# Kernel tuning notes

Measured on AMD Instinct MI355X. Metric: run time of the kernel, lower is better.

Reference implementation:

```python
import jax, jax.numpy as jnp
import numpy as np

N, C, NIRR, E = 2048, 128, 9, 10          # nodes, channels, sum(2l+1) of input irreps, num elements
DOUT = (1, 3)                              # output irrep dims for 128x0e + 128x1o
K3, K2, K1 = 4, 3, 2                       # number of CG paths per correlation order


def setup_inputs() -> dict:
    key = jax.random.key(0)
    ks = jax.random.split(key, 24)
    inp = {
        'node_feats': jax.random.normal(ks[0], (N, C, NIRR), jnp.float32),
        'node_attrs': jax.nn.one_hot(jax.random.randint(ks[1], (N,), 0, E), E, dtype=jnp.float32),
        'sc': jax.random.normal(ks[2], (N, C * sum(DOUT)), jnp.float32),
    }
    i = 3
    for li, d in enumerate(DOUT):
        # U tensors: fixed (buffer) generalized CG coupling tensors; sparse in e3nn,
        # here random dense stand-ins with the exact same shapes / contraction structure.
        inp[f'u3_l{li}'] = 0.1 * jax.random.normal(ks[i + 0], (d, NIRR, NIRR, NIRR, K3), jnp.float32)
        inp[f'u2_l{li}'] = 0.1 * jax.random.normal(ks[i + 1], (d, NIRR, NIRR, K2), jnp.float32)
        inp[f'u1_l{li}'] = 0.1 * jax.random.normal(ks[i + 2], (d, NIRR, K1), jnp.float32)
        s3, s2, s1 = 1.0 / np.sqrt(K3 * C), 1.0 / np.sqrt(K2 * C), 1.0 / np.sqrt(K1 * C)
        inp[f'w3_l{li}'] = s3 * jax.random.normal(ks[i + 3], (E, K3, C), jnp.float32)
        inp[f'w2_l{li}'] = s2 * jax.random.normal(ks[i + 4], (E, K2, C), jnp.float32)
        inp[f'w1_l{li}'] = s1 * jax.random.normal(ks[i + 5], (E, K1, C), jnp.float32)
        i += 6
    inp['lin_w0'] = jax.random.normal(ks[i], (C, C), jnp.float32)
    inp['lin_w1'] = jax.random.normal(ks[i + 1], (C, C), jnp.float32)
    return inp


def _contraction(x, y, u3, u2, u1, w3, w2, w1):
    # MACE Contraction: correlation-3 nested CG contraction for one output irrep.
    # x: [N,C,n], y: [N,E] one-hot, u_nu: [d, n*nu, k_nu], w_nu: [E, k_nu, C]
    wk3 = jnp.einsum('ekc,be->bkc', w3, y)                       # per-node path weights
    out = jnp.einsum('dpqik,bkc,bci->bcdpq', u3, wk3, x)         # main, nu=3
    out = jnp.einsum('dpik,ekc,be->bcdpi', u2, w2, y) + out      # add nu=2 weights
    out = jnp.einsum('bcdpi,bci->bcdp', out, x)                  # contract one feature index
    out = jnp.einsum('dik,ekc,be->bcdi', u1, w1, y) + out        # add nu=1 weights
    out = jnp.einsum('bcdi,bci->bcd', out, x)                    # [N,C,d]
    return out


def reference(node_feats, node_attrs, sc,
              u3_l0, u2_l0, u1_l0, w3_l0, w2_l0, w1_l0,
              u3_l1, u2_l1, u1_l1, w3_l1, w2_l1, w1_l1,
              lin_w0, lin_w1):
    f0 = _contraction(node_feats, node_attrs, u3_l0, u2_l0, u1_l0, w3_l0, w2_l0, w1_l0)  # [N,C,1]
    f1 = _contraction(node_feats, node_attrs, u3_l1, u2_l1, u1_l1, w3_l1, w2_l1, w1_l1)  # [N,C,3]
    inv_sqrt_c = 1.0 / np.sqrt(C).astype(np.float32)
    # o3.Linear: block-diagonal channel mixing per irrep, 1/sqrt(fan_in) normalization
    o0 = jnp.einsum('bim,ij->bjm', f0, lin_w0) * inv_sqrt_c
    o1 = jnp.einsum('bim,ij->bjm', f1, lin_w1) * inv_sqrt_c
    out = jnp.concatenate([o0.reshape(o0.shape[0], -1), o1.reshape(o1.shape[0], -1)], axis=-1)
    return out + sc
```

## Files before the change

kernel.cpp:

```cpp
#include <hip/hip_runtime.h>

#define N_NODES 2048
#define C_CH    128
#define NIRR    9
#define E_EL    10

#define NKT 14
#define UTAB_HALVES (NKT * 512)

typedef _Float16 f16x8 __attribute__((ext_vector_type(8)));
typedef float   f32x16 __attribute__((ext_vector_type(16)));
typedef float   f32x4u __attribute__((ext_vector_type(4), aligned(4)));
typedef float   pf2    __attribute__((ext_vector_type(2)));

struct MonoTab {
    unsigned char a[224], b2[224], c[224], msk[224];
};
constexpr MonoTab makeMono() {
    MonoTab m{};
    int s3 = 0;
    for (int p = 0; p < 9; p++)
        for (int q = p; q < 9; q++)
            for (int i = q; i < 9; i++) { m.a[s3] = p; m.b2[s3] = q; m.c[s3] = i; m.msk[s3] = 1; s3++; }
    int s2 = 0;
    for (int p = 0; p < 9; p++)
        for (int q = p; q < 9; q++) { m.a[165 + s2] = p; m.b2[165 + s2] = q; m.c[165 + s2] = 9; m.msk[165 + s2] = 1; s2++; }
    for (int p = 0; p < 9; p++) { m.a[210 + p] = p; m.b2[210 + p] = 9; m.c[210 + p] = 9; m.msk[210 + p] = 1; }
    for (int k = 219; k < 224; k++) { m.a[k] = 9; m.b2[k] = 9; m.c[k] = 9; m.msk[k] = 0; }
    return m;
}
constexpr MonoTab MT = makeMono();

__global__ __launch_bounds__(256) void build_utab_kernel(
    const float* __restrict__ u3_l0, const float* __restrict__ u2_l0, const float* __restrict__ u1_l0,
    const float* __restrict__ u3_l1, const float* __restrict__ u2_l1, const float* __restrict__ u1_l1,
    _Float16* __restrict__ Utab, float* __restrict__ us1f)
{
    int t = blockIdx.x * 256 + threadIdx.x;
    if (t < UTAB_HALVES) {
        int kt = t / 512, idx = t % 512;
        int lane = idx >> 3, j = idx & 7;
        int m = lane & 31, g = lane >> 5;
        int k = kt * 16 + g * 8 + j;
        float v = 0.f;
        if (m < 16) {
            int ds = m >> 2, kk = m & 3;
            if (k < 165) {
                int pp = 0, qq = 0, ii = 0, cnt = 0;
                for (int p = 0; p < 9; p++)
                    for (int q = p; q < 9; q++)
                        for (int i = q; i < 9; i++) {
                            if (cnt == k) { pp = p; qq = q; ii = i; }
                            cnt++;
                        }
                const float* u = (ds == 0) ? u3_l0 : (u3_l1 + (ds - 1) * 2916);
                int perm[6][3] = {{pp,qq,ii},{pp,ii,qq},{qq,pp,ii},{qq,ii,pp},{ii,pp,qq},{ii,qq,pp}};
                float acc = 0.f;
                #pragma unroll
                for (int w = 0; w < 6; w++)
                    acc += u[((perm[w][0] * 9 + perm[w][1]) * 9 + perm[w][2]) * 4 + kk];
                float mult = (pp == qq && qq == ii) ? 6.f : ((pp == qq || qq == ii) ? 2.f : 1.f);
                v = acc / mult;
            }
        } else if (m < 28) {
            int r = m - 16, ds = r / 3, kk = r % 3;
            if (k >= 165 && k < 210) {
                int s = k - 165;
                int pp = 0, qq = 0, cnt = 0;
                for (int p = 0; p < 9; p++)
                    for (int q = p; q < 9; q++) {
                        if (cnt == s) { pp = p; qq = q; }
                        cnt++;
                    }
                const float* u = (ds == 0) ? u2_l0 : (u2_l1 + (ds - 1) * 243);
                float acc = u[(pp * 9 + qq) * 3 + kk] + u[(qq * 9 + pp) * 3 + kk];
                v = (pp == qq) ? acc * 0.5f : acc;
            }
        } else {
            int r = m - 28, ds = r >> 1, kk = r & 1;
            if (k >= 210 && k < 219) {
                int p = k - 210;
                v = (ds == 0) ? u1_l0[p * 2 + kk] : u1_l1[(0 * 9 + p) * 2 + kk];
            }
        }
        Utab[t] = (_Float16)v;
    } else if (t < UTAB_HALVES + 72) {
        int q = t - UTAB_HALVES;
        int ds = q / 18, rem = q % 18, p = rem >> 1, kk = rem & 1;
        us1f[q] = (ds == 0) ? u1_l0[p * 2 + kk] : u1_l1[((ds - 1) * 9 + p) * 2 + kk];
    }
}

__global__ __launch_bounds__(256, 2) void fused_kernel(
    const float* __restrict__ x, const float* __restrict__ y,
    const _Float16* __restrict__ Utab, const float* __restrict__ us1f,
    const float* __restrict__ w3_l0, const float* __restrict__ w2_l0, const float* __restrict__ w1_l0,
    const float* __restrict__ w3_l1, const float* __restrict__ w2_l1, const float* __restrict__ w1_l1,
    const float* __restrict__ lw0, const float* __restrict__ lw1,
    const float* __restrict__ sc, float* __restrict__ out)
{
    __shared__ float fs[4][4][132];
    int tid = threadIdx.x;
    int lane = tid & 63;
    int wid = tid >> 6;
    int n = lane & 31, g = lane >> 5;
    int b0 = blockIdx.x * 4;
    int b = b0 + wid;

    const f16x8* U8 = (const f16x8*)Utab;

    int e = 0;
    #pragma unroll
    for (int k = 1; k < E_EL; k++)
        if (y[b * E_EL + k] > 0.5f) e = k;
    e = __builtin_amdgcn_readfirstlane(e);

    #pragma unroll 1
    for (int tl = 0; tl < 4; tl++) {
        int c = tl * 32 + n;
        const float* xp = x + ((size_t)b * C_CH + c) * NIRR;
        f32x4u xa = *(const f32x4u*)xp;
        f32x4u xb = *(const f32x4u*)(xp + 4);
        float xv10[10] = {xa[0], xa[1], xa[2], xa[3], xb[0], xb[1], xb[2], xb[3], xp[8], 1.f};

        f32x16 acc;
        #pragma unroll
        for (int z = 0; z < 16; z++) acc[z] = 0.f;

        #pragma unroll
        for (int kt = 0; kt < NKT; kt++) {
            f16x8 af = U8[kt * 64 + lane];
            float mf[8];
            if (g == 0) {
                #pragma unroll
                for (int j = 0; j < 8; j++) {
                    const int k = kt * 16 + j;
                    mf[j] = MT.msk[k] ? xv10[MT.a[k]] * xv10[MT.b2[k]] * xv10[MT.c[k]] : 0.f;
                }
            } else {
                #pragma unroll
                for (int j = 0; j < 8; j++) {
                    const int k = kt * 16 + 8 + j;
                    mf[j] = MT.msk[k] ? xv10[MT.a[k]] * xv10[MT.b2[k]] * xv10[MT.c[k]] : 0.f;
                }
            }
            f16x8 bf;
            #pragma unroll
            for (int j = 0; j < 8; j++) bf[j] = (_Float16)mf[j];
            acc = __builtin_amdgcn_mfma_f32_32x32x16_f16(af, bf, acc, 0, 0, 0);
        }

        float G[32];
        #pragma unroll
        for (int reg = 0; reg < 16; reg++) {
            float own = acc[reg];
            float oth = __shfl_xor(own, 32, 64);
            int base = (reg & 3) + 8 * (reg >> 2);
            G[base]     = (g == 0) ? own : oth;
            G[base + 4] = (g == 0) ? oth : own;
        }

        float G1hi[4];
        #pragma unroll
        for (int dd = 0; dd < 2; dd++) {
            #pragma unroll
            for (int kk = 0; kk < 2; kk++) {
                float a = 0.f;
                #pragma unroll
                for (int p = 0; p < 9; p++)
                    a += us1f[(2 + dd) * 18 + p * 2 + kk] * xv10[p];
                G1hi[dd * 2 + kk] = a;
            }
        }

        float f0;
        {
            float a = 0.f;
            #pragma unroll
            for (int kk = 0; kk < 4; kk++) a += w3_l0[(e * 4 + kk) * 128 + c] * G[kk];
            #pragma unroll
            for (int kk = 0; kk < 3; kk++) a += w2_l0[(e * 3 + kk) * 128 + c] * G[16 + kk];
            #pragma unroll
            for (int kk = 0; kk < 2; kk++) a += w1_l0[(e * 2 + kk) * 128 + c] * G[28 + kk];
            f0 = a;
        }
        float f123[3];
        #pragma unroll
        for (int ds = 1; ds < 4; ds++) {
            float a = 0.f;
            #pragma unroll
            for (int kk = 0; kk < 4; kk++) a += w3_l1[(e * 4 + kk) * 128 + c] * G[ds * 4 + kk];
            #pragma unroll
            for (int kk = 0; kk < 3; kk++) a += w2_l1[(e * 3 + kk) * 128 + c] * G[16 + ds * 3 + kk];
            #pragma unroll
            for (int kk = 0; kk < 2; kk++) {
                float g1 = (ds < 2) ? G[28 + ds * 2 + kk] : G1hi[(ds - 2) * 2 + kk];
                a += w1_l1[(e * 2 + kk) * 128 + c] * g1;
            }
            f123[ds - 1] = a;
        }
        if (g == 0) {
            fs[wid][0][c] = f0;
            fs[wid][1][c] = f123[0];
            fs[wid][2][c] = f123[1];
            fs[wid][3][c] = f123[2];
        }
    }
    __syncthreads();

    {
        int p = tid >> 7;
        int t = tid & 127;
        int sel, m = 0, j0;
        const float4* W4;
        bool isl0 = (t < 32);
        if (isl0) { sel = 0; j0 = 4 * t; W4 = (const float4*)lw0; }
        else {
            int idx = t - 32;
            m = idx >> 5;
            j0 = 4 * (idx & 31);
            sel = 1 + m;
            W4 = (const float4*)lw1;
        }
        int wbase = j0 >> 2;

        pf2 a01A = {0.f, 0.f}, a23A = {0.f, 0.f};
        pf2 a01B = {0.f, 0.f}, a23B = {0.f, 0.f};
        #pragma unroll 4
        for (int ib = 0; ib < 32; ib++) {
            float4 fA = *(const float4*)&fs[p][sel][4 * ib];
            float4 fB = *(const float4*)&fs[p + 2][sel][4 * ib];
            float frA[4] = {fA.x, fA.y, fA.z, fA.w};
            float frB[4] = {fB.x, fB.y, fB.z, fB.w};
            #pragma unroll
            for (int r = 0; r < 4; r++) {
                float4 w = W4[(4 * ib + r) * 32 + wbase];
                pf2 wlo = {w.x, w.y};
                pf2 whi = {w.z, w.w};
                pf2 fra = {frA[r], frA[r]};
                pf2 frb = {frB[r], frB[r]};
                a01A = __builtin_elementwise_fma(wlo, fra, a01A);
                a23A = __builtin_elementwise_fma(whi, fra, a23A);
                a01B = __builtin_elementwise_fma(wlo, frb, a01B);
                a23B = __builtin_elementwise_fma(whi, frb, a23B);
            }
        }
        const float inv_sqrt_c = 0.08838834764831845f;

        {
            int bb = b0 + p;
            float a0 = a01A[0], a1 = a01A[1], a2 = a23A[0], a3 = a23A[1];
            if (isl0) {
                size_t o = (size_t)bb * 512 + j0;
                float4 s = *(const float4*)(sc + o);
                float4 rr;
                rr.x = a0 * inv_sqrt_c + s.x;
                rr.y = a1 * inv_sqrt_c + s.y;
                rr.z = a2 * inv_sqrt_c + s.z;
                rr.w = a3 * inv_sqrt_c + s.w;
                *(float4*)(out + o) = rr;
            } else {
                float av[4] = {a0, a1, a2, a3};
                #pragma unroll
                for (int jj = 0; jj < 4; jj++) {
                    size_t o = (size_t)bb * 512 + 128 + 3 * (j0 + jj) + m;
                    out[o] = av[jj] * inv_sqrt_c + sc[o];
                }
            }
        }
        {
            int bb = b0 + p + 2;
            float a0 = a01B[0], a1 = a01B[1], a2 = a23B[0], a3 = a23B[1];
            if (isl0) {
                size_t o = (size_t)bb * 512 + j0;
                float4 s = *(const float4*)(sc + o);
                float4 rr;
                rr.x = a0 * inv_sqrt_c + s.x;
                rr.y = a1 * inv_sqrt_c + s.y;
                rr.z = a2 * inv_sqrt_c + s.z;
                rr.w = a3 * inv_sqrt_c + s.w;
                *(float4*)(out + o) = rr;
            } else {
                float av[4] = {a0, a1, a2, a3};
                #pragma unroll
                for (int jj = 0; jj < 4; jj++) {
                    size_t o = (size_t)bb * 512 + 128 + 3 * (j0 + jj) + m;
                    out[o] = av[jj] * inv_sqrt_c + sc[o];
                }
            }
        }
    }
}

extern "C" void kernel_launch(void* const* d_in, const int* in_sizes, int n_in,
                              void* d_out, int out_size, void* d_ws, size_t ws_size,
                              hipStream_t stream) {
    const float* x     = (const float*)d_in[0];
    const float* y     = (const float*)d_in[1];
    const float* sc    = (const float*)d_in[2];
    const float* u3_l0 = (const float*)d_in[3];
    const float* u2_l0 = (const float*)d_in[4];
    const float* u1_l0 = (const float*)d_in[5];
    const float* w3_l0 = (const float*)d_in[6];
    const float* w2_l0 = (const float*)d_in[7];
    const float* w1_l0 = (const float*)d_in[8];
    const float* u3_l1 = (const float*)d_in[9];
    const float* u2_l1 = (const float*)d_in[10];
    const float* u1_l1 = (const float*)d_in[11];
    const float* w3_l1 = (const float*)d_in[12];
    const float* w2_l1 = (const float*)d_in[13];
    const float* w1_l1 = (const float*)d_in[14];
    const float* lw0   = (const float*)d_in[15];
    const float* lw1   = (const float*)d_in[16];
    float* out = (float*)d_out;

    _Float16* Utab = (_Float16*)d_ws;
    float* us1f = (float*)((char*)d_ws + UTAB_HALVES * 2);

    build_utab_kernel<<<(UTAB_HALVES + 72 + 255) / 256, 256, 0, stream>>>(
        u3_l0, u2_l0, u1_l0, u3_l1, u2_l1, u1_l1, Utab, us1f);
    fused_kernel<<<N_NODES / 4, 256, 0, stream>>>(
        x, y, Utab, us1f,
        w3_l0, w2_l0, w1_l0, w3_l1, w2_l1, w1_l1,
        lw0, lw1, sc, out);
}
```

Before: 116.0 us.

## Split per-node channel tiles across two waves and reduce MFMA outputs via partial sums

```diff
diff --git a/kernel.cpp b/kernel.cpp
--- a/kernel.cpp
+++ b/kernel.cpp
@@ -46,13 +46,7 @@
         if (m < 16) {
             int ds = m >> 2, kk = m & 3;
             if (k < 165) {
-                int pp = 0, qq = 0, ii = 0, cnt = 0;
-                for (int p = 0; p < 9; p++)
-                    for (int q = p; q < 9; q++)
-                        for (int i = q; i < 9; i++) {
-                            if (cnt == k) { pp = p; qq = q; ii = i; }
-                            cnt++;
-                        }
+                int pp = MT.a[k], qq = MT.b2[k], ii = MT.c[k];
                 const float* u = (ds == 0) ? u3_l0 : (u3_l1 + (ds - 1) * 2916);
                 int perm[6][3] = {{pp,qq,ii},{pp,ii,qq},{qq,pp,ii},{qq,ii,pp},{ii,pp,qq},{ii,qq,pp}};
                 float acc = 0.f;
@@ -65,13 +59,7 @@
         } else if (m < 28) {
             int r = m - 16, ds = r / 3, kk = r % 3;
             if (k >= 165 && k < 210) {
-                int s = k - 165;
-                int pp = 0, qq = 0, cnt = 0;
-                for (int p = 0; p < 9; p++)
-                    for (int q = p; q < 9; q++) {
-                        if (cnt == s) { pp = p; qq = q; }
-                        cnt++;
-                    }
+                int pp = MT.a[k], qq = MT.b2[k];
                 const float* u = (ds == 0) ? u2_l0 : (u2_l1 + (ds - 1) * 243);
                 float acc = u[(pp * 9 + qq) * 3 + kk] + u[(qq * 9 + pp) * 3 + kk];
                 v = (pp == qq) ? acc * 0.5f : acc;
@@ -91,7 +79,7 @@
     }
 }
 
-__global__ __launch_bounds__(256, 2) void fused_kernel(
+__global__ __launch_bounds__(512, 4) void fused_kernel(
     const float* __restrict__ x, const float* __restrict__ y,
     const _Float16* __restrict__ Utab, const float* __restrict__ us1f,
     const float* __restrict__ w3_l0, const float* __restrict__ w2_l0, const float* __restrict__ w1_l0,
@@ -105,7 +93,9 @@
     int wid = tid >> 6;
     int n = lane & 31, g = lane >> 5;
     int b0 = blockIdx.x * 4;
-    int b = b0 + wid;
+    int nd = wid >> 1;
+    int b = b0 + nd;
+    int th = wid & 1;
 
     const f16x8* U8 = (const f16x8*)Utab;
 
@@ -116,8 +106,8 @@
     e = __builtin_amdgcn_readfirstlane(e);
 
     #pragma unroll 1
-    for (int tl = 0; tl < 4; tl++) {
-        int c = tl * 32 + n;
+    for (int tl2 = 0; tl2 < 2; tl2++) {
+        int c = (th * 2 + tl2) * 32 + n;
         const float* xp = x + ((size_t)b * C_CH + c) * NIRR;
         f32x4u xa = *(const f32x4u*)xp;
         f32x4u xb = *(const f32x4u*)(xp + 4);
@@ -150,16 +140,6 @@
             acc = __builtin_amdgcn_mfma_f32_32x32x16_f16(af, bf, acc, 0, 0, 0);
         }
 
-        float G[32];
-        #pragma unroll
-        for (int reg = 0; reg < 16; reg++) {
-            float own = acc[reg];
-            float oth = __shfl_xor(own, 32, 64);
-            int base = (reg & 3) + 8 * (reg >> 2);
-            G[base]     = (g == 0) ? own : oth;
-            G[base + 4] = (g == 0) ? oth : own;
-        }
-
         float G1hi[4];
         #pragma unroll
         for (int dd = 0; dd < 2; dd++) {
@@ -173,42 +153,57 @@
             }
         }
 
-        float f0;
-        {
-            float a = 0.f;
-            #pragma unroll
-            for (int kk = 0; kk < 4; kk++) a += w3_l0[(e * 4 + kk) * 128 + c] * G[kk];
-            #pragma unroll
-            for (int kk = 0; kk < 3; kk++) a += w2_l0[(e * 3 + kk) * 128 + c] * G[16 + kk];
-            #pragma unroll
-            for (int kk = 0; kk < 2; kk++) a += w1_l0[(e * 2 + kk) * 128 + c] * G[28 + kk];
-            f0 = a;
-        }
-        float f123[3];
-        #pragma unroll
-        for (int ds = 1; ds < 4; ds++) {
-            float a = 0.f;
-            #pragma unroll
-            for (int kk = 0; kk < 4; kk++) a += w3_l1[(e * 4 + kk) * 128 + c] * G[ds * 4 + kk];
-            #pragma unroll
-            for (int kk = 0; kk < 3; kk++) a += w2_l1[(e * 3 + kk) * 128 + c] * G[16 + ds * 3 + kk];
-            #pragma unroll
-            for (int kk = 0; kk < 2; kk++) {
-                float g1 = (ds < 2) ? G[28 + ds * 2 + kk] : G1hi[(ds - 2) * 2 + kk];
-                a += w1_l1[(e * 2 + kk) * 128 + c] * g1;
-            }
-            f123[ds - 1] = a;
-        }
+        float p0, p1, p2, p3;
         if (g == 0) {
-            fs[wid][0][c] = f0;
-            fs[wid][1][c] = f123[0];
-            fs[wid][2][c] = f123[1];
-            fs[wid][3][c] = f123[2];
+            p0 = 0.f;
+            #pragma unroll
+            for (int kk = 0; kk < 4; kk++) p0 += w3_l0[(e * 4 + kk) * 128 + c] * acc[kk];
+            #pragma unroll
+            for (int kk = 0; kk < 3; kk++) p0 += w2_l0[(e * 3 + kk) * 128 + c] * acc[8 + kk];
+            p1 = w2_l1[(e * 3 + 0) * 128 + c] * acc[11];
+            p2 = 0.f;
+            #pragma unroll
+            for (int kk = 0; kk < 4; kk++) p2 += w3_l1[(e * 4 + kk) * 128 + c] * acc[4 + kk];
+            p2 += w2_l1[(e * 3 + 2) * 128 + c] * acc[12];
+            p3 = 0.f;
+            #pragma unroll
+            for (int kk = 0; kk < 3; kk++) p3 += w2_l1[(e * 3 + kk) * 128 + c] * acc[13 + kk];
+            #pragma unroll
+            for (int kk = 0; kk < 2; kk++) p3 += w1_l1[(e * 2 + kk) * 128 + c] * G1hi[2 + kk];
+        } else {
+            p0 = w1_l0[(e * 2 + 0) * 128 + c] * acc[12]
+               + w1_l0[(e * 2 + 1) * 128 + c] * acc[13];
+            p1 = 0.f;
+            #pragma unroll
+            for (int kk = 0; kk < 4; kk++) p1 += w3_l1[(e * 4 + kk) * 128 + c] * acc[kk];
+            p1 += w2_l1[(e * 3 + 1) * 128 + c] * acc[8];
+            p1 += w2_l1[(e * 3 + 2) * 128 + c] * acc[9];
+            #pragma unroll
+            for (int kk = 0; kk < 2; kk++) p1 += w1_l1[(e * 2 + kk) * 128 + c] * acc[14 + kk];
+            p2 = w2_l1[(e * 3 + 0) * 128 + c] * acc[10]
+               + w2_l1[(e * 3 + 1) * 128 + c] * acc[11];
+            #pragma unroll
+            for (int kk = 0; kk < 2; kk++) p2 += w1_l1[(e * 2 + kk) * 128 + c] * G1hi[kk];
+            p3 = 0.f;
+            #pragma unroll
+            for (int kk = 0; kk < 4; kk++) p3 += w3_l1[(e * 4 + kk) * 128 + c] * acc[4 + kk];
+        }
+        float f0 = p0 + __shfl_xor(p0, 32, 64);
+        float f1 = p1 + __shfl_xor(p1, 32, 64);
+        float f2 = p2 + __shfl_xor(p2, 32, 64);
+        float f3 = p3 + __shfl_xor(p3, 32, 64);
+
+        if (g == 0) {
+            fs[nd][0][c] = f0;
+            fs[nd][1][c] = f1;
+        } else {
+            fs[nd][2][c] = f2;
+            fs[nd][3][c] = f3;
         }
     }
     __syncthreads();
 
-    {
+    if (tid < 256) {
         int p = tid >> 7;
         int t = tid & 127;
         int sel, m = 0, j0;
@@ -319,7 +314,7 @@
 
     build_utab_kernel<<<(UTAB_HALVES + 72 + 255) / 256, 256, 0, stream>>>(
         u3_l0, u2_l0, u1_l0, u3_l1, u2_l1, u1_l1, Utab, us1f);
-    fused_kernel<<<N_NODES / 4, 256, 0, stream>>>(
+    fused_kernel<<<N_NODES / 4, 512, 0, stream>>>(
         x, y, Utab, us1f,
         w3_l0, w2_l0, w1_l0, w3_l1, w2_l1, w1_l1,
         lw0, lw1, sc, out);
```

Result: no change. 117.1 us (+1.0%).
